# Kernel tuning notes

Measured on AMD Instinct MI355X. Metric: run time of the kernel, lower is better.

The kernel has to match this reference:

```python
import jax, jax.numpy as jnp
import numpy as np

B, N, D, S = 16, 128, 128, 128   # batch, n_nodes, node/edge feat dim, state_dim
MP_INT = 256
UP_INT = 256
EPS = 1e-3  # keras BatchNormalization default epsilon


def _mlp(x, W1, b1, W2, b2):
    # Dense(relu) -> Dense(relu)
    h = jax.nn.relu(x @ W1 + b1)
    return jax.nn.relu(h @ W2 + b2)


def setup_inputs() -> dict:
    key = jax.random.key(0)
    ks = jax.random.split(key, 16)
    g = lambda k, shape: jax.random.normal(k, shape, dtype=jnp.float32) * 0.05
    nodes = jax.random.normal(ks[0], (B, N, D), dtype=jnp.float32)
    edges = jax.random.normal(ks[1], (B, N * N, D), dtype=jnp.float32)
    mask = (jax.random.uniform(ks[2], (B, N * N, 1)) > 0.5).astype(jnp.float32)
    return {
        "nodes": nodes, "edges": edges, "mask": mask,
        # Adj_Updater_1: concat(node_i, node_j, edge_ij) -> UP_INT -> S
        "W1a": g(ks[3], (3 * D, UP_INT)), "b1a": jnp.zeros((UP_INT,), jnp.float32),
        "W2a": g(ks[4], (UP_INT, S)), "b2a": jnp.zeros((S,), jnp.float32),
        # Message_Passer_1: concat(node_i, node_j, new_edge) -> MP_INT -> S
        "W1m": g(ks[5], (2 * D + S, MP_INT)), "b1m": jnp.zeros((MP_INT,), jnp.float32),
        "W2m": g(ks[6], (MP_INT, S)), "b2m": jnp.zeros((S,), jnp.float32),
        # Update_Func_1: concat(old_state, agg_messages) -> UP_INT -> S
        "W1u": g(ks[7], (D + S, UP_INT)), "b1u": jnp.zeros((UP_INT,), jnp.float32),
        "W2u": g(ks[8], (UP_INT, S)), "b2u": jnp.zeros((S,), jnp.float32),
        # BatchNorm (inference mode: moving stats) for nodes and edges
        "gamma_n": jnp.ones((S,), jnp.float32), "beta_n": jnp.zeros((S,), jnp.float32),
        "mean_n": jnp.zeros((S,), jnp.float32), "var_n": jnp.ones((S,), jnp.float32),
        "gamma_e": jnp.ones((S,), jnp.float32), "beta_e": jnp.zeros((S,), jnp.float32),
        "mean_e": jnp.zeros((S,), jnp.float32), "var_e": jnp.ones((S,), jnp.float32),
    }


def reference(nodes, edges, mask,
              W1a, b1a, W2a, b2a,
              W1m, b1m, W2m, b2m,
              W1u, b1u, W2u, b2u,
              gamma_n, beta_n, mean_n, var_n,
              gamma_e, beta_e, mean_e, var_e):
    b, n, d = nodes.shape
    # tf.tile(nodes,[1,n,1]): row p*n+q -> nodes[q]  (state_i)
    state_i = jnp.broadcast_to(nodes[:, None, :, :], (b, n, n, d)).reshape(b, n * n, d)
    # reshape(tile(nodes,[1,1,n])): row p*n+q -> nodes[p]  (state_j)
    state_j = jnp.broadcast_to(nodes[:, :, None, :], (b, n, n, d)).reshape(b, n * n, d)

    new_edges = _mlp(jnp.concatenate([state_i, state_j, edges], axis=-1), W1a, b1a, W2a, b2a)
    new_edges = new_edges * mask

    messages = _mlp(jnp.concatenate([state_i, state_j, new_edges], axis=-1), W1m, b1m, W2m, b2m)
    masked = (messages * mask).reshape(b, n, n, -1)
    agg_m = masked.sum(axis=2)  # reduce over axis 2 as in Message_Agg

    state_1 = _mlp(jnp.concatenate([nodes, agg_m], axis=-1), W1u, b1u, W2u, b2u)

    bn = lambda x, g_, b_, m_, v_: g_ * (x - m_) * jax.lax.rsqrt(v_ + EPS) + b_
    nodes_out = bn(state_1, gamma_n, beta_n, mean_n, var_n)
    edges_out = bn(new_edges, gamma_e, beta_e, mean_e, var_e)
    return nodes_out, edges_out
```

## Files before the change

kernel.cpp:

```cpp
#include <hip/hip_runtime.h>
#include <hip/hip_bf16.h>
#include <cstdint>
#include <cstddef>


typedef __attribute__((ext_vector_type(8))) __bf16 bf16x8;
typedef __attribute__((ext_vector_type(4))) float f32x4;

#define GLDS(gp, lp)                                                        \
  __builtin_amdgcn_global_load_lds(                                         \
      (const __attribute__((address_space(1))) void*)(gp),                  \
      (__attribute__((address_space(3))) void*)(lp), 16, 0, 0)

__device__ inline bf16x8 load8_cvt(const float* __restrict__ p) {
  const float4 a = *(const float4*)p;
  const float4 b = *(const float4*)(p + 4);
  bf16x8 r;
  r[0] = (__bf16)a.x; r[1] = (__bf16)a.y; r[2] = (__bf16)a.z; r[3] = (__bf16)a.w;
  r[4] = (__bf16)b.x; r[5] = (__bf16)b.y; r[6] = (__bf16)b.z; r[7] = (__bf16)b.w;
  return r;
}

__global__ void __launch_bounds__(256) proj_kernel(
    const float* __restrict__ nodes, const float* __restrict__ W1a,
    const float* __restrict__ b1a, const float* __restrict__ W1m,
    const float* __restrict__ b1m, float* __restrict__ outP) {
  __shared__ float x[8][128];
  const int mat = blockIdx.y;
  const int t = threadIdx.x;
  const float* W = (mat < 2 ? W1a : W1m) + ((mat & 1) ? 128 * 256 : 0);
  float* out = outP + (size_t)mat * (2048 * 256);
  const int r0 = blockIdx.x * 8;
  for (int i = t; i < 1024; i += 256)
    x[i >> 7][i & 127] = nodes[r0 * 128 + i];
  __syncthreads();
  float bv = 0.f;
  if (mat == 1) bv = b1a[t];
  if (mat == 3) bv = b1m[t];
  float acc[8];
#pragma unroll
  for (int r = 0; r < 8; ++r) acc[r] = bv;
  for (int k = 0; k < 128; ++k) {
    float w = W[k * 256 + t];
#pragma unroll
    for (int r = 0; r < 8; ++r) acc[r] += x[r][k] * w;
  }
  for (int r = 0; r < 8; ++r) out[(size_t)(r0 + r) * 256 + t] = acc[r];
}

__global__ void __launch_bounds__(256) wswz_kernel(
    const float* __restrict__ W1a, const float* __restrict__ W2a,
    const float* __restrict__ W1m, const float* __restrict__ W2m,
    __hip_bfloat16* __restrict__ dstp) {
  __bf16* dst = (__bf16*)dstp;
  const int mat = blockIdx.y;
  const float* src;
  __bf16* d;
  int nsh;
  if (mat == 0)      { src = W1a + 65536; d = dst;         nsh = 8; }
  else if (mat == 1) { src = W2a;         d = dst + 32768; nsh = 7; }
  else if (mat == 2) { src = W1m + 65536; d = dst + 65536; nsh = 8; }
  else               { src = W2m;         d = dst + 98304; nsh = 7; }
  const int nmask = (1 << nsh) - 1;
  const int base = (blockIdx.x * 256 + threadIdx.x) * 4;
#pragma unroll
  for (int i = 0; i < 4; ++i) {
    int s = base + i;
    int k = s >> nsh, n = s & nmask;
    float v = src[s];
    int g = k >> 3;
    if (nsh == 8) {
      int gs = (g & 8) | ((g ^ n) & 7);
      d[n * 128 + gs * 8 + (k & 7)] = (__bf16)v;
    } else {
      int gs = (g ^ n) & 7;
      d[((k >> 6) << 13) + (n << 6) + (gs << 3) + (k & 7)] = (__bf16)v;
    }
  }
}

__global__ void __launch_bounds__(256, 3) fused_mlp_kernel(
    const float* __restrict__ edges, const float* __restrict__ mask,
    const float* __restrict__ b2a, const float* __restrict__ b2m,
    const float* __restrict__ ge, const float* __restrict__ be,
    const float* __restrict__ me, const float* __restrict__ ve,
    const float* __restrict__ Pa, const float* __restrict__ Qab,
    const float* __restrict__ Pm, const float* __restrict__ Qmb,
    const __hip_bfloat16* __restrict__ Wsw, float* __restrict__ edges_out,
    float* __restrict__ agg) {
  __shared__ __align__(16) char sArena[49152];
  char* const sW1h = sArena;
  char* const sW2h = sArena + 16384;
  char* const sH1q = sArena + 32768;
  float* const sAgg = (float*)(sArena + 32768);
  __shared__ float sQ[256];
  __shared__ float sB2a[128];
  __shared__ float sB2m[128];
  __shared__ float sMask[128];
  __shared__ float sScE[128];
  __shared__ float sShE[128];

  const int t = threadIdx.x;
  const int lane = t & 63, wv = t >> 6;
  const int cl = lane & 15, qd = lane >> 4;
  const int m0 = wv * 32;

  const int bb = blockIdx.x >> 7;
  const int p = blockIdx.x & 127;

  if (t < 128) {
    sB2a[t] = b2a[t];
    sB2m[t] = b2m[t];
    float sc = ge[t] * rsqrtf(ve[t] + 1e-3f);
    sScE[t] = sc;
    sShE[t] = be[t] - me[t] * sc;
    sMask[t] = mask[(bb << 14) + (p << 7) + t];
  }
  sQ[t] = Qab[((bb << 7) + p) * 256 + t];
  __syncthreads();

  const float* Xb = edges + ((size_t)((bb << 14) + (p << 7)) << 7);
  bf16x8 xf[2][4];
#pragma unroll
  for (int mt = 0; mt < 2; ++mt)
#pragma unroll
    for (int ks = 0; ks < 4; ++ks)
      xf[mt][ks] = load8_cvt(Xb + (m0 + mt * 16 + cl) * 128 + ks * 32 + qd * 8);

  f32x4 ne[2][8];
#pragma unroll
  for (int mt = 0; mt < 2; ++mt)
#pragma unroll
    for (int nt = 0; nt < 8; ++nt) {
      float bv = sB2a[nt * 16 + cl];
      ne[mt][nt] = (f32x4){bv, bv, bv, bv};
    }

  const char* gW1e = (const char*)Wsw;
  const char* gW2e = (const char*)(Wsw + 32768);

  for (int h = 0; h < 4; ++h) {
    __syncthreads();
    {
      const char* gW1 = gW1e + h * 16384;
      const char* gW2 = gW2e + h * 16384;
      for (int o = wv * 1024; o < 16384; o += 4096) {
        GLDS(gW1 + o + lane * 16, sW1h + o);
        GLDS(gW2 + o + lane * 16, sW2h + o);
      }
    }
    f32x4 a1[2][4];
#pragma unroll
    for (int mt = 0; mt < 2; ++mt)
#pragma unroll
      for (int nt = 0; nt < 4; ++nt) {
        const int col = h * 64 + nt * 16 + cl;
        const int mrow = m0 + mt * 16 + qd * 4;
        const float qv = sQ[col];
        const float* pa = Pa + (size_t)((bb << 7) + mrow) * 256 + col;
        a1[mt][nt] = (f32x4){pa[0] + qv, pa[256] + qv, pa[512] + qv, pa[768] + qv};
      }
    __syncthreads();
#pragma unroll
    for (int ks = 0; ks < 4; ++ks)
#pragma unroll
      for (int nt = 0; nt < 4; ++nt) {
        const int nl = nt * 16 + cl;
        const int g = ks * 4 + qd;
        const int gs = (g & 8) | ((g ^ nl) & 7);
        bf16x8 bw = *(const bf16x8*)(sW1h + nl * 256 + gs * 16);
        a1[0][nt] = __builtin_amdgcn_mfma_f32_16x16x32_bf16(xf[0][ks], bw, a1[0][nt], 0, 0, 0);
        a1[1][nt] = __builtin_amdgcn_mfma_f32_16x16x32_bf16(xf[1][ks], bw, a1[1][nt], 0, 0, 0);
      }
#pragma unroll
    for (int mt = 0; mt < 2; ++mt)
#pragma unroll
      for (int nt = 0; nt < 4; ++nt) {
        const int kq = nt * 16 + cl;
#pragma unroll
        for (int r = 0; r < 4; ++r) {
          const int m = m0 + mt * 16 + qd * 4 + r;
          float v = a1[mt][nt][r];
          v = v > 0.f ? v : 0.f;
          const int gs = ((kq >> 3) ^ m) & 7;
          *(__bf16*)(sH1q + m * 128 + gs * 16 + (kq & 7) * 2) = (__bf16)v;
        }
      }
    __syncthreads();
    bf16x8 hf[2][2];
#pragma unroll
    for (int mt = 0; mt < 2; ++mt)
#pragma unroll
      for (int ks = 0; ks < 2; ++ks) {
        const int m = m0 + mt * 16 + cl;
        const int g = ks * 4 + qd;
        const int gs = (g ^ m) & 7;
        hf[mt][ks] = *(const bf16x8*)(sH1q + m * 128 + gs * 16);
      }
#pragma unroll
    for (int ks = 0; ks < 2; ++ks)
#pragma unroll
      for (int nt = 0; nt < 8; ++nt) {
        const int n = nt * 16 + cl;
        const int g = ks * 4 + qd;
        const int gs = (g ^ n) & 7;
        bf16x8 bw = *(const bf16x8*)(sW2h + n * 128 + gs * 16);
        ne[0][nt] = __builtin_amdgcn_mfma_f32_16x16x32_bf16(hf[0][ks], bw, ne[0][nt], 0, 0, 0);
        ne[1][nt] = __builtin_amdgcn_mfma_f32_16x16x32_bf16(hf[1][ks], bw, ne[1][nt], 0, 0, 0);
      }
  }

  __syncthreads();
  sQ[t] = Qmb[((bb << 7) + p) * 256 + t];
  {
    float* Ob = edges_out + ((size_t)((bb << 14) + (p << 7)) << 7);
#pragma unroll
    for (int mt = 0; mt < 2; ++mt)
#pragma unroll
      for (int nt = 0; nt < 8; ++nt) {
        const int col = nt * 16 + cl;
        const float sc = sScE[col], sh = sShE[col];
        char* const buf = (nt & 4) ? sW2h : sW1h;
        const int kq = col & 63;
#pragma unroll
        for (int r = 0; r < 4; ++r) {
          const int m = m0 + mt * 16 + qd * 4 + r;
          float v = ne[mt][nt][r];
          v = v > 0.f ? v : 0.f;
          const float e = v * sMask[m];
          Ob[m * 128 + col] = e * sc + sh;
          const int gs = ((kq >> 3) ^ m) & 7;
          *(__bf16*)(buf + m * 128 + gs * 16 + (kq & 7) * 2) = (__bf16)e;
        }
      }
  }
  __syncthreads();

  bf16x8 xf2[2][4];
#pragma unroll
  for (int mt = 0; mt < 2; ++mt)
#pragma unroll
    for (int ks = 0; ks < 4; ++ks) {
      const int m = m0 + mt * 16 + cl;
      const int g = (ks & 1) * 4 + qd;
      const int gs = (g ^ m) & 7;
      const char* buf = (ks & 2) ? sW2h : sW1h;
      xf2[mt][ks] = *(const bf16x8*)(buf + m * 128 + gs * 16);
    }

  f32x4 ms[2][8];
#pragma unroll
  for (int mt = 0; mt < 2; ++mt)
#pragma unroll
    for (int nt = 0; nt < 8; ++nt) {
      float bv = sB2m[nt * 16 + cl];
      ms[mt][nt] = (f32x4){bv, bv, bv, bv};
    }

  const char* gW1m = (const char*)(Wsw + 65536);
  const char* gW2m = (const char*)(Wsw + 98304);

  for (int h = 0; h < 4; ++h) {
    __syncthreads();
    {
      const char* gW1 = gW1m + h * 16384;
      const char* gW2 = gW2m + h * 16384;
      for (int o = wv * 1024; o < 16384; o += 4096) {
        GLDS(gW1 + o + lane * 16, sW1h + o);
        GLDS(gW2 + o + lane * 16, sW2h + o);
      }
    }
    f32x4 a1[2][4];
#pragma unroll
    for (int mt = 0; mt < 2; ++mt)
#pragma unroll
      for (int nt = 0; nt < 4; ++nt) {
        const int col = h * 64 + nt * 16 + cl;
        const int mrow = m0 + mt * 16 + qd * 4;
        const float qv = sQ[col];
        const float* pa = Pm + (size_t)((bb << 7) + mrow) * 256 + col;
        a1[mt][nt] = (f32x4){pa[0] + qv, pa[256] + qv, pa[512] + qv, pa[768] + qv};
      }
    __syncthreads();
#pragma unroll
    for (int ks = 0; ks < 4; ++ks)
#pragma unroll
      for (int nt = 0; nt < 4; ++nt) {
        const int nl = nt * 16 + cl;
        const int g = ks * 4 + qd;
        const int gs = (g & 8) | ((g ^ nl) & 7);
        bf16x8 bw = *(const bf16x8*)(sW1h + nl * 256 + gs * 16);
        a1[0][nt] = __builtin_amdgcn_mfma_f32_16x16x32_bf16(xf2[0][ks], bw, a1[0][nt], 0, 0, 0);
        a1[1][nt] = __builtin_amdgcn_mfma_f32_16x16x32_bf16(xf2[1][ks], bw, a1[1][nt], 0, 0, 0);
      }
#pragma unroll
    for (int mt = 0; mt < 2; ++mt)
#pragma unroll
      for (int nt = 0; nt < 4; ++nt) {
        const int kq = nt * 16 + cl;
#pragma unroll
        for (int r = 0; r < 4; ++r) {
          const int m = m0 + mt * 16 + qd * 4 + r;
          float v = a1[mt][nt][r];
          v = v > 0.f ? v : 0.f;
          const int gs = ((kq >> 3) ^ m) & 7;
          *(__bf16*)(sH1q + m * 128 + gs * 16 + (kq & 7) * 2) = (__bf16)v;
        }
      }
    __syncthreads();
    bf16x8 hf[2][2];
#pragma unroll
    for (int mt = 0; mt < 2; ++mt)
#pragma unroll
      for (int ks = 0; ks < 2; ++ks) {
        const int m = m0 + mt * 16 + cl;
        const int g = ks * 4 + qd;
        const int gs = (g ^ m) & 7;
        hf[mt][ks] = *(const bf16x8*)(sH1q + m * 128 + gs * 16);
      }
#pragma unroll
    for (int ks = 0; ks < 2; ++ks)
#pragma unroll
      for (int nt = 0; nt < 8; ++nt) {
        const int n = nt * 16 + cl;
        const int g = ks * 4 + qd;
        const int gs = (g ^ n) & 7;
        bf16x8 bw = *(const bf16x8*)(sW2h + n * 128 + gs * 16);
        ms[0][nt] = __builtin_amdgcn_mfma_f32_16x16x32_bf16(hf[0][ks], bw, ms[0][nt], 0, 0, 0);
        ms[1][nt] = __builtin_amdgcn_mfma_f32_16x16x32_bf16(hf[1][ks], bw, ms[1][nt], 0, 0, 0);
      }
  }

  float ss[8];
#pragma unroll
  for (int nt = 0; nt < 8; ++nt) {
    float s = 0.f;
#pragma unroll
    for (int mt = 0; mt < 2; ++mt)
#pragma unroll
      for (int r = 0; r < 4; ++r) {
        const int m = m0 + mt * 16 + qd * 4 + r;
        float v = ms[mt][nt][r];
        v = v > 0.f ? v : 0.f;
        s += v * sMask[m];
      }
    s += __shfl_xor(s, 16);
    s += __shfl_xor(s, 32);
    ss[nt] = s;
  }
  __syncthreads();
  if (lane < 16) {
#pragma unroll
    for (int nt = 0; nt < 8; ++nt) sAgg[wv * 128 + nt * 16 + lane] = ss[nt];
  }
  __syncthreads();
  if (t < 128)
    agg[((bb << 7) + p) * 128 + t] =
        sAgg[t] + sAgg[128 + t] + sAgg[256 + t] + sAgg[384 + t];
}

__global__ void __launch_bounds__(256) update_kernel(
    const float* __restrict__ nodes, const float* __restrict__ agg,
    const float* __restrict__ W1u, const float* __restrict__ b1u,
    const float* __restrict__ W2u, const float* __restrict__ b2u,
    const float* __restrict__ gn, const float* __restrict__ btn,
    const float* __restrict__ mn, const float* __restrict__ vn,
    float* __restrict__ out) {
  __shared__ float x[8][256];
  __shared__ float hh[8][256];
  const int t = threadIdx.x;
  const int r0 = blockIdx.x * 8;
  for (int i = t; i < 2048; i += 256) {
    int r = i >> 8, c = i & 255;
    x[r][c] = (c < 128) ? nodes[(r0 + r) * 128 + c] : agg[(r0 + r) * 128 + (c - 128)];
  }
  __syncthreads();
  float acc[8];
  {
    float bv = b1u[t];
#pragma unroll
    for (int r = 0; r < 8; ++r) acc[r] = bv;
  }
  for (int k = 0; k < 256; ++k) {
    float w = W1u[k * 256 + t];
#pragma unroll
    for (int r = 0; r < 8; ++r) acc[r] += x[r][k] * w;
  }
#pragma unroll
  for (int r = 0; r < 8; ++r) hh[r][t] = acc[r] > 0.f ? acc[r] : 0.f;
  __syncthreads();
  const int j = t & 127, half = t >> 7;
  float a2[4];
  {
    float bv = b2u[j];
#pragma unroll
    for (int r = 0; r < 4; ++r) a2[r] = bv;
  }
  for (int k = 0; k < 256; ++k) {
    float w = W2u[k * 128 + j];
#pragma unroll
    for (int r = 0; r < 4; ++r) a2[r] += hh[half * 4 + r][k] * w;
  }
  float sc = gn[j] * rsqrtf(vn[j] + 1e-3f);
  float sh = btn[j] - mn[j] * sc;
#pragma unroll
  for (int r = 0; r < 4; ++r) {
    float v = a2[r] > 0.f ? a2[r] : 0.f;
    out[(r0 + half * 4 + r) * 128 + j] = v * sc + sh;
  }
}

extern "C" void kernel_launch(void* const* d_in, const int* in_sizes, int n_in,
                              void* d_out, int out_size, void* d_ws,
                              size_t ws_size, hipStream_t stream) {
  (void)in_sizes; (void)n_in; (void)out_size; (void)ws_size;
  const float* nodes = (const float*)d_in[0];
  const float* edges = (const float*)d_in[1];
  const float* mask = (const float*)d_in[2];
  const float* W1a = (const float*)d_in[3];
  const float* b1a = (const float*)d_in[4];
  const float* W2a = (const float*)d_in[5];
  const float* b2a = (const float*)d_in[6];
  const float* W1m = (const float*)d_in[7];
  const float* b1m = (const float*)d_in[8];
  const float* W2m = (const float*)d_in[9];
  const float* b2m = (const float*)d_in[10];
  const float* W1u = (const float*)d_in[11];
  const float* b1u = (const float*)d_in[12];
  const float* W2u = (const float*)d_in[13];
  const float* b2u = (const float*)d_in[14];
  const float* gn = (const float*)d_in[15];
  const float* btn = (const float*)d_in[16];
  const float* mn = (const float*)d_in[17];
  const float* vn = (const float*)d_in[18];
  const float* ge = (const float*)d_in[19];
  const float* be = (const float*)d_in[20];
  const float* me = (const float*)d_in[21];
  const float* ve = (const float*)d_in[22];

  float* out_nodes = (float*)d_out;
  float* out_edges = (float*)d_out + 262144;

  char* ws = (char*)d_ws;
  float* Pa = (float*)(ws);
  float* Qab = (float*)(ws + ((size_t)1 << 21));
  float* Pm = (float*)(ws + ((size_t)2 << 21));
  float* Qmb = (float*)(ws + ((size_t)3 << 21));
  float* agg = (float*)(ws + ((size_t)4 << 21));
  __hip_bfloat16* Wsw = (__hip_bfloat16*)(ws + ((size_t)4 << 21) + ((size_t)1 << 20));

  proj_kernel<<<dim3(256, 4), 256, 0, stream>>>(nodes, W1a, b1a, W1m, b1m, Pa);
  wswz_kernel<<<dim3(32, 4), 256, 0, stream>>>(W1a, W2a, W1m, W2m, Wsw);
  fused_mlp_kernel<<<2048, 256, 0, stream>>>(edges, mask, b2a, b2m, ge, be, me,
                                             ve, Pa, Qab, Pm, Qmb, Wsw,
                                             out_edges, agg);
  update_kernel<<<256, 256, 0, stream>>>(nodes, agg, W1u, b1u, W2u, b2u, gn, btn,
                                         mn, vn, out_nodes);
}
```

Baseline: 524.6 us.

## Split edge rows across two blocks and read weights directly from global/L2

Each block now handles 64 of the 128 neighbor rows (16 per wave) instead of 128, doubling the grid to 4096 blocks. The aggregated message is combined with atomicAdd into an agg buffer that proj_kernel now zeroes. Weights are no longer staged into LDS via global_load_lds. MFMA B-fragments are loaded straight from a plain transposed bf16 layout in global memory, and the hidden activations are double-buffered in a smaller LDS area. This is meant to cut LDS footprint and barriers and to raise parallelism, at the cost of more L2 weight traffic, float atomics, and occupancy hint lowered to 2.

```diff
diff --git a/kernel.cpp b/kernel.cpp
--- a/kernel.cpp
+++ b/kernel.cpp
@@ -5,12 +5,8 @@
 
 
 typedef __attribute__((ext_vector_type(8))) __bf16 bf16x8;
+typedef __attribute__((ext_vector_type(4))) __bf16 bf16x4;
 typedef __attribute__((ext_vector_type(4))) float f32x4;
-
-#define GLDS(gp, lp)                                                        \
-  __builtin_amdgcn_global_load_lds(                                         \
-      (const __attribute__((address_space(1))) void*)(gp),                  \
-      (__attribute__((address_space(3))) void*)(lp), 16, 0, 0)
 
 __device__ inline bf16x8 load8_cvt(const float* __restrict__ p) {
   const float4 a = *(const float4*)p;
@@ -24,10 +20,15 @@
 __global__ void __launch_bounds__(256) proj_kernel(
     const float* __restrict__ nodes, const float* __restrict__ W1a,
     const float* __restrict__ b1a, const float* __restrict__ W1m,
-    const float* __restrict__ b1m, float* __restrict__ outP) {
+    const float* __restrict__ b1m, float* __restrict__ outP,
+    float* __restrict__ agg) {
   __shared__ float x[8][128];
   const int mat = blockIdx.y;
   const int t = threadIdx.x;
+  if (mat == 0) {
+#pragma unroll
+    for (int i = 0; i < 4; ++i) agg[blockIdx.x * 1024 + i * 256 + t] = 0.f;
+  }
   const float* W = (mat < 2 ? W1a : W1m) + ((mat & 1) ? 128 * 256 : 0);
   float* out = outP + (size_t)mat * (2048 * 256);
   const int r0 = blockIdx.x * 8;
@@ -56,30 +57,26 @@
   const int mat = blockIdx.y;
   const float* src;
   __bf16* d;
-  int nsh;
-  if (mat == 0)      { src = W1a + 65536; d = dst;         nsh = 8; }
-  else if (mat == 1) { src = W2a;         d = dst + 32768; nsh = 7; }
-  else if (mat == 2) { src = W1m + 65536; d = dst + 65536; nsh = 8; }
-  else               { src = W2m;         d = dst + 98304; nsh = 7; }
-  const int nmask = (1 << nsh) - 1;
+  if (mat == 0)      { src = W1a + 65536; d = dst; }
+  else if (mat == 1) { src = W2a;         d = dst + 32768; }
+  else if (mat == 2) { src = W1m + 65536; d = dst + 65536; }
+  else               { src = W2m;         d = dst + 98304; }
   const int base = (blockIdx.x * 256 + threadIdx.x) * 4;
-#pragma unroll
-  for (int i = 0; i < 4; ++i) {
-    int s = base + i;
-    int k = s >> nsh, n = s & nmask;
-    float v = src[s];
-    int g = k >> 3;
-    if (nsh == 8) {
-      int gs = (g & 8) | ((g ^ n) & 7);
-      d[n * 128 + gs * 8 + (k & 7)] = (__bf16)v;
-    } else {
-      int gs = (g ^ n) & 7;
-      d[((k >> 6) << 13) + (n << 6) + (gs << 3) + (k & 7)] = (__bf16)v;
-    }
-  }
-}
-
-__global__ void __launch_bounds__(256, 3) fused_mlp_kernel(
+  bf16x4 v;
+  if (mat == 0 || mat == 2) {
+    const int n = base >> 7, k0 = base & 127;
+#pragma unroll
+    for (int i = 0; i < 4; ++i) v[i] = (__bf16)src[(k0 + i) * 256 + n];
+    *(bf16x4*)(d + n * 128 + k0) = v;
+  } else {
+    const int n = base >> 8, k0 = base & 255;
+#pragma unroll
+    for (int i = 0; i < 4; ++i) v[i] = (__bf16)src[(k0 + i) * 128 + n];
+    *(bf16x4*)(d + n * 256 + k0) = v;
+  }
+}
+
+__global__ void __launch_bounds__(256, 2) fused_mlp_kernel(
     const float* __restrict__ edges, const float* __restrict__ mask,
     const float* __restrict__ b2a, const float* __restrict__ b2m,
     const float* __restrict__ ge, const float* __restrict__ be,
@@ -88,25 +85,19 @@
     const float* __restrict__ Pm, const float* __restrict__ Qmb,
     const __hip_bfloat16* __restrict__ Wsw, float* __restrict__ edges_out,
     float* __restrict__ agg) {
-  __shared__ __align__(16) char sArena[49152];
-  char* const sW1h = sArena;
-  char* const sW2h = sArena + 16384;
-  char* const sH1q = sArena + 32768;
-  float* const sAgg = (float*)(sArena + 32768);
+  __shared__ __align__(16) char sH[2][8192];
   __shared__ float sQ[256];
-  __shared__ float sB2a[128];
-  __shared__ float sB2m[128];
-  __shared__ float sMask[128];
-  __shared__ float sScE[128];
-  __shared__ float sShE[128];
+  __shared__ float sB2a[128], sB2m[128], sScE[128], sShE[128];
+  __shared__ float sMask[64];
 
   const int t = threadIdx.x;
   const int lane = t & 63, wv = t >> 6;
   const int cl = lane & 15, qd = lane >> 4;
-  const int m0 = wv * 32;
-
-  const int bb = blockIdx.x >> 7;
-  const int p = blockIdx.x & 127;
+  const int m0 = wv << 4;
+
+  const int bb = blockIdx.x >> 8;
+  const int p = (blockIdx.x >> 1) & 127;
+  const int q0 = (blockIdx.x & 1) << 6;
 
   if (t < 128) {
     sB2a[t] = b2a[t];
@@ -114,220 +105,167 @@
     float sc = ge[t] * rsqrtf(ve[t] + 1e-3f);
     sScE[t] = sc;
     sShE[t] = be[t] - me[t] * sc;
-    sMask[t] = mask[(bb << 14) + (p << 7) + t];
-  }
+  }
+  if (t < 64) sMask[t] = mask[(bb << 14) + (p << 7) + q0 + t];
   sQ[t] = Qab[((bb << 7) + p) * 256 + t];
   __syncthreads();
 
-  const float* Xb = edges + ((size_t)((bb << 14) + (p << 7)) << 7);
-  bf16x8 xf[2][4];
-#pragma unroll
-  for (int mt = 0; mt < 2; ++mt)
+  const float* Xb = edges + ((size_t)((bb << 14) + (p << 7) + q0) << 7);
+  bf16x8 xf[4];
+#pragma unroll
+  for (int ks = 0; ks < 4; ++ks)
+    xf[ks] = load8_cvt(Xb + (m0 + cl) * 128 + ks * 32 + qd * 8);
+
+  f32x4 ne[8];
+#pragma unroll
+  for (int nt = 0; nt < 8; ++nt) {
+    float bv = sB2a[nt * 16 + cl];
+    ne[nt] = (f32x4){bv, bv, bv, bv};
+  }
+
+  const __bf16* w1 = (const __bf16*)Wsw;
+  const __bf16* w2 = (const __bf16*)Wsw + 32768;
+  const float* Prow = Pa + (size_t)((bb << 7) + q0 + m0 + qd * 4) * 256;
+
+#pragma unroll 1
+  for (int h = 0; h < 4; ++h) {
+    f32x4 a1[4];
+#pragma unroll
+    for (int nt = 0; nt < 4; ++nt) {
+      const int col = h * 64 + nt * 16 + cl;
+      const float qv = sQ[col];
+      a1[nt] = (f32x4){Prow[col] + qv, Prow[256 + col] + qv,
+                       Prow[512 + col] + qv, Prow[768 + col] + qv};
+    }
 #pragma unroll
     for (int ks = 0; ks < 4; ++ks)
-      xf[mt][ks] = load8_cvt(Xb + (m0 + mt * 16 + cl) * 128 + ks * 32 + qd * 8);
-
-  f32x4 ne[2][8];
-#pragma unroll
-  for (int mt = 0; mt < 2; ++mt)
-#pragma unroll
-    for (int nt = 0; nt < 8; ++nt) {
-      float bv = sB2a[nt * 16 + cl];
-      ne[mt][nt] = (f32x4){bv, bv, bv, bv};
-    }
-
-  const char* gW1e = (const char*)Wsw;
-  const char* gW2e = (const char*)(Wsw + 32768);
-
-  for (int h = 0; h < 4; ++h) {
+#pragma unroll
+      for (int nt = 0; nt < 4; ++nt) {
+        bf16x8 bw = *(const bf16x8*)(w1 + (h * 64 + nt * 16 + cl) * 128 +
+                                     ks * 32 + qd * 8);
+        a1[nt] = __builtin_amdgcn_mfma_f32_16x16x32_bf16(xf[ks], bw, a1[nt], 0, 0, 0);
+      }
+    char* const Hb = sH[h & 1];
+#pragma unroll
+    for (int nt = 0; nt < 4; ++nt) {
+      const int kq = nt * 16 + cl;
+#pragma unroll
+      for (int r = 0; r < 4; ++r) {
+        const int m = m0 + qd * 4 + r;
+        float v = a1[nt][r];
+        v = v > 0.f ? v : 0.f;
+        *(__bf16*)(Hb + m * 128 + ((((kq >> 3) ^ m) & 7) << 4) + ((kq & 7) << 1)) =
+            (__bf16)v;
+      }
+    }
     __syncthreads();
-    {
-      const char* gW1 = gW1e + h * 16384;
-      const char* gW2 = gW2e + h * 16384;
-      for (int o = wv * 1024; o < 16384; o += 4096) {
-        GLDS(gW1 + o + lane * 16, sW1h + o);
-        GLDS(gW2 + o + lane * 16, sW2h + o);
-      }
-    }
-    f32x4 a1[2][4];
-#pragma unroll
-    for (int mt = 0; mt < 2; ++mt)
-#pragma unroll
-      for (int nt = 0; nt < 4; ++nt) {
-        const int col = h * 64 + nt * 16 + cl;
-        const int mrow = m0 + mt * 16 + qd * 4;
-        const float qv = sQ[col];
-        const float* pa = Pa + (size_t)((bb << 7) + mrow) * 256 + col;
-        a1[mt][nt] = (f32x4){pa[0] + qv, pa[256] + qv, pa[512] + qv, pa[768] + qv};
-      }
-    __syncthreads();
-#pragma unroll
-    for (int ks = 0; ks < 4; ++ks)
-#pragma unroll
-      for (int nt = 0; nt < 4; ++nt) {
-        const int nl = nt * 16 + cl;
-        const int g = ks * 4 + qd;
-        const int gs = (g & 8) | ((g ^ nl) & 7);
-        bf16x8 bw = *(const bf16x8*)(sW1h + nl * 256 + gs * 16);
-        a1[0][nt] = __builtin_amdgcn_mfma_f32_16x16x32_bf16(xf[0][ks], bw, a1[0][nt], 0, 0, 0);
-        a1[1][nt] = __builtin_amdgcn_mfma_f32_16x16x32_bf16(xf[1][ks], bw, a1[1][nt], 0, 0, 0);
-      }
-#pragma unroll
-    for (int mt = 0; mt < 2; ++mt)
-#pragma unroll
-      for (int nt = 0; nt < 4; ++nt) {
-        const int kq = nt * 16 + cl;
-#pragma unroll
-        for (int r = 0; r < 4; ++r) {
-          const int m = m0 + mt * 16 + qd * 4 + r;
-          float v = a1[mt][nt][r];
-          v = v > 0.f ? v : 0.f;
-          const int gs = ((kq >> 3) ^ m) & 7;
-          *(__bf16*)(sH1q + m * 128 + gs * 16 + (kq & 7) * 2) = (__bf16)v;
-        }
-      }
-    __syncthreads();
-    bf16x8 hf[2][2];
-#pragma unroll
-    for (int mt = 0; mt < 2; ++mt)
-#pragma unroll
-      for (int ks = 0; ks < 2; ++ks) {
-        const int m = m0 + mt * 16 + cl;
-        const int g = ks * 4 + qd;
-        const int gs = (g ^ m) & 7;
-        hf[mt][ks] = *(const bf16x8*)(sH1q + m * 128 + gs * 16);
-      }
+    bf16x8 hf[2];
+#pragma unroll
+    for (int ks = 0; ks < 2; ++ks) {
+      const int m = m0 + cl;
+      const int gs = ((ks * 4 + qd) ^ m) & 7;
+      hf[ks] = *(const bf16x8*)(Hb + m * 128 + gs * 16);
+    }
 #pragma unroll
     for (int ks = 0; ks < 2; ++ks)
 #pragma unroll
       for (int nt = 0; nt < 8; ++nt) {
-        const int n = nt * 16 + cl;
-        const int g = ks * 4 + qd;
-        const int gs = (g ^ n) & 7;
-        bf16x8 bw = *(const bf16x8*)(sW2h + n * 128 + gs * 16);
-        ne[0][nt] = __builtin_amdgcn_mfma_f32_16x16x32_bf16(hf[0][ks], bw, ne[0][nt], 0, 0, 0);
-        ne[1][nt] = __builtin_amdgcn_mfma_f32_16x16x32_bf16(hf[1][ks], bw, ne[1][nt], 0, 0, 0);
+        bf16x8 bw = *(const bf16x8*)(w2 + (nt * 16 + cl) * 256 + h * 64 +
+                                     ks * 32 + qd * 8);
+        ne[nt] = __builtin_amdgcn_mfma_f32_16x16x32_bf16(hf[ks], bw, ne[nt], 0, 0, 0);
       }
   }
 
   __syncthreads();
   sQ[t] = Qmb[((bb << 7) + p) * 256 + t];
   {
-    float* Ob = edges_out + ((size_t)((bb << 14) + (p << 7)) << 7);
-#pragma unroll
-    for (int mt = 0; mt < 2; ++mt)
+    float* Ob = edges_out + ((size_t)((bb << 14) + (p << 7) + q0) << 7);
+#pragma unroll
+    for (int nt = 0; nt < 8; ++nt) {
+      const int col = nt * 16 + cl;
+      const float sc = sScE[col], sh = sShE[col];
+      char* const buf = sH[(nt >> 2) & 1];
+      const int kq = col & 63;
+#pragma unroll
+      for (int r = 0; r < 4; ++r) {
+        const int m = m0 + qd * 4 + r;
+        float v = ne[nt][r];
+        v = v > 0.f ? v : 0.f;
+        const float e = v * sMask[m];
+        Ob[m * 128 + col] = e * sc + sh;
+        *(__bf16*)(buf + m * 128 + ((((kq >> 3) ^ m) & 7) << 4) + ((kq & 7) << 1)) =
+            (__bf16)e;
+      }
+    }
+  }
+  __syncthreads();
+
+  bf16x8 xf2[4];
+#pragma unroll
+  for (int ks = 0; ks < 4; ++ks) {
+    const int m = m0 + cl;
+    const int gs = (((ks & 1) * 4 + qd) ^ m) & 7;
+    xf2[ks] = *(const bf16x8*)(sH[(ks >> 1) & 1] + m * 128 + gs * 16);
+  }
+  __syncthreads();
+
+  f32x4 ms[8];
+#pragma unroll
+  for (int nt = 0; nt < 8; ++nt) {
+    float bv = sB2m[nt * 16 + cl];
+    ms[nt] = (f32x4){bv, bv, bv, bv};
+  }
+
+  const __bf16* w1m = (const __bf16*)Wsw + 65536;
+  const __bf16* w2m = (const __bf16*)Wsw + 98304;
+  const float* Pmrow = Pm + (size_t)((bb << 7) + q0 + m0 + qd * 4) * 256;
+
+#pragma unroll 1
+  for (int h = 0; h < 4; ++h) {
+    f32x4 a1[4];
+#pragma unroll
+    for (int nt = 0; nt < 4; ++nt) {
+      const int col = h * 64 + nt * 16 + cl;
+      const float qv = sQ[col];
+      a1[nt] = (f32x4){Pmrow[col] + qv, Pmrow[256 + col] + qv,
+                       Pmrow[512 + col] + qv, Pmrow[768 + col] + qv};
+    }
+#pragma unroll
+    for (int ks = 0; ks < 4; ++ks)
+#pragma unroll
+      for (int nt = 0; nt < 4; ++nt) {
+        bf16x8 bw = *(const bf16x8*)(w1m + (h * 64 + nt * 16 + cl) * 128 +
+                                     ks * 32 + qd * 8);
+        a1[nt] = __builtin_amdgcn_mfma_f32_16x16x32_bf16(xf2[ks], bw, a1[nt], 0, 0, 0);
+      }
+    char* const Hb = sH[h & 1];
+#pragma unroll
+    for (int nt = 0; nt < 4; ++nt) {
+      const int kq = nt * 16 + cl;
+#pragma unroll
+      for (int r = 0; r < 4; ++r) {
+        const int m = m0 + qd * 4 + r;
+        float v = a1[nt][r];
+        v = v > 0.f ? v : 0.f;
+        *(__bf16*)(Hb + m * 128 + ((((kq >> 3) ^ m) & 7) << 4) + ((kq & 7) << 1)) =
+            (__bf16)v;
+      }
+    }
+    __syncthreads();
+    bf16x8 hf[2];
+#pragma unroll
+    for (int ks = 0; ks < 2; ++ks) {
+      const int m = m0 + cl;
+      const int gs = ((ks * 4 + qd) ^ m) & 7;
+      hf[ks] = *(const bf16x8*)(Hb + m * 128 + gs * 16);
+    }
+#pragma unroll
+    for (int ks = 0; ks < 2; ++ks)
 #pragma unroll
       for (int nt = 0; nt < 8; ++nt) {
-        const int col = nt * 16 + cl;
-        const float sc = sScE[col], sh = sShE[col];
-        char* const buf = (nt & 4) ? sW2h : sW1h;
-        const int kq = col & 63;
-#pragma unroll
-        for (int r = 0; r < 4; ++r) {
-          const int m = m0 + mt * 16 + qd * 4 + r;
-          float v = ne[mt][nt][r];
-          v = v > 0.f ? v : 0.f;
-          const float e = v * sMask[m];
-          Ob[m * 128 + col] = e * sc + sh;
-          const int gs = ((kq >> 3) ^ m) & 7;
-          *(__bf16*)(buf + m * 128 + gs * 16 + (kq & 7) * 2) = (__bf16)e;
-        }
-      }
-  }
-  __syncthreads();
-
-  bf16x8 xf2[2][4];
-#pragma unroll
-  for (int mt = 0; mt < 2; ++mt)
-#pragma unroll
-    for (int ks = 0; ks < 4; ++ks) {
-      const int m = m0 + mt * 16 + cl;
-      const int g = (ks & 1) * 4 + qd;
-      const int gs = (g ^ m) & 7;
-      const char* buf = (ks & 2) ? sW2h : sW1h;
-      xf2[mt][ks] = *(const bf16x8*)(buf + m * 128 + gs * 16);
-    }
-
-  f32x4 ms[2][8];
-#pragma unroll
-  for (int mt = 0; mt < 2; ++mt)
-#pragma unroll
-    for (int nt = 0; nt < 8; ++nt) {
-      float bv = sB2m[nt * 16 + cl];
-      ms[mt][nt] = (f32x4){bv, bv, bv, bv};
-    }
-
-  const char* gW1m = (const char*)(Wsw + 65536);
-  const char* gW2m = (const char*)(Wsw + 98304);
-
-  for (int h = 0; h < 4; ++h) {
-    __syncthreads();
-    {
-      const char* gW1 = gW1m + h * 16384;
-      const char* gW2 = gW2m + h * 16384;
-      for (int o = wv * 1024; o < 16384; o += 4096) {
-        GLDS(gW1 + o + lane * 16, sW1h + o);
-        GLDS(gW2 + o + lane * 16, sW2h + o);
-      }
-    }
-    f32x4 a1[2][4];
-#pragma unroll
-    for (int mt = 0; mt < 2; ++mt)
-#pragma unroll
-      for (int nt = 0; nt < 4; ++nt) {
-        const int col = h * 64 + nt * 16 + cl;
-        const int mrow = m0 + mt * 16 + qd * 4;
-        const float qv = sQ[col];
-        const float* pa = Pm + (size_t)((bb << 7) + mrow) * 256 + col;
-        a1[mt][nt] = (f32x4){pa[0] + qv, pa[256] + qv, pa[512] + qv, pa[768] + qv};
-      }
-    __syncthreads();
-#pragma unroll
-    for (int ks = 0; ks < 4; ++ks)
-#pragma unroll
-      for (int nt = 0; nt < 4; ++nt) {
-        const int nl = nt * 16 + cl;
-        const int g = ks * 4 + qd;
-        const int gs = (g & 8) | ((g ^ nl) & 7);
-        bf16x8 bw = *(const bf16x8*)(sW1h + nl * 256 + gs * 16);
-        a1[0][nt] = __builtin_amdgcn_mfma_f32_16x16x32_bf16(xf2[0][ks], bw, a1[0][nt], 0, 0, 0);
-        a1[1][nt] = __builtin_amdgcn_mfma_f32_16x16x32_bf16(xf2[1][ks], bw, a1[1][nt], 0, 0, 0);
-      }
-#pragma unroll
-    for (int mt = 0; mt < 2; ++mt)
-#pragma unroll
-      for (int nt = 0; nt < 4; ++nt) {
-        const int kq = nt * 16 + cl;
-#pragma unroll
-        for (int r = 0; r < 4; ++r) {
-          const int m = m0 + mt * 16 + qd * 4 + r;
-          float v = a1[mt][nt][r];
-          v = v > 0.f ? v : 0.f;
-          const int gs = ((kq >> 3) ^ m) & 7;
-          *(__bf16*)(sH1q + m * 128 + gs * 16 + (kq & 7) * 2) = (__bf16)v;
-        }
-      }
-    __syncthreads();
-    bf16x8 hf[2][2];
-#pragma unroll
-    for (int mt = 0; mt < 2; ++mt)
-#pragma unroll
-      for (int ks = 0; ks < 2; ++ks) {
-        const int m = m0 + mt * 16 + cl;
-        const int g = ks * 4 + qd;
-        const int gs = (g ^ m) & 7;
-        hf[mt][ks] = *(const bf16x8*)(sH1q + m * 128 + gs * 16);
-      }
-#pragma unroll
-    for (int ks = 0; ks < 2; ++ks)
-#pragma unroll
-      for (int nt = 0; nt < 8; ++nt) {
-        const int n = nt * 16 + cl;
-        const int g = ks * 4 + qd;
-        const int gs = (g ^ n) & 7;
-        bf16x8 bw = *(const bf16x8*)(sW2h + n * 128 + gs * 16);
-        ms[0][nt] = __builtin_amdgcn_mfma_f32_16x16x32_bf16(hf[0][ks], bw, ms[0][nt], 0, 0, 0);
-        ms[1][nt] = __builtin_amdgcn_mfma_f32_16x16x32_bf16(hf[1][ks], bw, ms[1][nt], 0, 0, 0);
+        bf16x8 bw = *(const bf16x8*)(w2m + (nt * 16 + cl) * 256 + h * 64 +
+                                     ks * 32 + qd * 8);
+        ms[nt] = __builtin_amdgcn_mfma_f32_16x16x32_bf16(hf[ks], bw, ms[nt], 0, 0, 0);
       }
   }
 
@@ -336,27 +274,26 @@
   for (int nt = 0; nt < 8; ++nt) {
     float s = 0.f;
 #pragma unroll
-    for (int mt = 0; mt < 2; ++mt)
-#pragma unroll
-      for (int r = 0; r < 4; ++r) {
-        const int m = m0 + mt * 16 + qd * 4 + r;
-        float v = ms[mt][nt][r];
-        v = v > 0.f ? v : 0.f;
-        s += v * sMask[m];
-      }
+    for (int r = 0; r < 4; ++r) {
+      const int m = m0 + qd * 4 + r;
+      float v = ms[nt][r];
+      v = v > 0.f ? v : 0.f;
+      s += v * sMask[m];
+    }
     s += __shfl_xor(s, 16);
     s += __shfl_xor(s, 32);
     ss[nt] = s;
   }
   __syncthreads();
+  float* const sAgg = (float*)sH[0];
   if (lane < 16) {
 #pragma unroll
     for (int nt = 0; nt < 8; ++nt) sAgg[wv * 128 + nt * 16 + lane] = ss[nt];
   }
   __syncthreads();
   if (t < 128)
-    agg[((bb << 7) + p) * 128 + t] =
-        sAgg[t] + sAgg[128 + t] + sAgg[256 + t] + sAgg[384 + t];
+    atomicAdd(&agg[((bb << 7) + p) * 128 + t],
+              sAgg[t] + sAgg[128 + t] + sAgg[256 + t] + sAgg[384 + t]);
 }
 
 __global__ void __launch_bounds__(256) update_kernel(
@@ -449,9 +386,9 @@
   float* agg = (float*)(ws + ((size_t)4 << 21));
   __hip_bfloat16* Wsw = (__hip_bfloat16*)(ws + ((size_t)4 << 21) + ((size_t)1 << 20));
 
-  proj_kernel<<<dim3(256, 4), 256, 0, stream>>>(nodes, W1a, b1a, W1m, b1m, Pa);
+  proj_kernel<<<dim3(256, 4), 256, 0, stream>>>(nodes, W1a, b1a, W1m, b1m, Pa, agg);
   wswz_kernel<<<dim3(32, 4), 256, 0, stream>>>(W1a, W2a, W1m, W2m, Wsw);
-  fused_mlp_kernel<<<2048, 256, 0, stream>>>(edges, mask, b2a, b2m, ge, be, me,
+  fused_mlp_kernel<<<4096, 256, 0, stream>>>(edges, mask, b2a, b2m, ge, be, me,
                                              ve, Pa, Qab, Pm, Qmb, Wsw,
                                              out_edges, agg);
   update_kernel<<<256, 256, 0, stream>>>(nodes, agg, W1u, b1u, W2u, b2u, gn, btn,
```

New measurement: 836.8 us. +59.5%, slower.
